# Kernel optimization log

Measured on AMD Instinct MI355X. Metric: run time of the kernel, lower is better.

The kernel has to match this reference:

```python
import jax, jax.numpy as jnp
import numpy as np

# Mixtral attention constants
H, KVH, HD = 32, 8, 128      # query heads, kv heads, head dim
WINDOW = 512                  # sliding window
THETA = 1e6                   # rope theta
B, S = 4, 1024                # batch (sequences), tokens per sequence
BS, NUM_BLOCKS = 64, 72       # paged cache block size / total blocks
DM = H * HD                   # 4096 hidden size


def rotate_half(x):
    x1, x2 = jnp.split(x, 2, axis=-1)
    return jnp.concatenate((-x2, x1), axis=-1)


def setup_inputs() -> dict:
    key = jax.random.key(0)
    ks = jax.random.split(key, 6)
    hidden_states = jax.random.normal(ks[0], (B * S, DM), dtype=jnp.float32)
    Wq = jax.random.normal(ks[1], (DM, H * HD), dtype=jnp.float32) * 0.02
    Wk = jax.random.normal(ks[2], (DM, KVH * HD), dtype=jnp.float32) * 0.02
    Wv = jax.random.normal(ks[3], (DM, KVH * HD), dtype=jnp.float32) * 0.02
    Wo = jax.random.normal(ks[4], (H * HD, DM), dtype=jnp.float32) * 0.02
    k_cache = jnp.zeros((NUM_BLOCKS, BS, KVH, HD), dtype=jnp.float32)
    v_cache = jnp.zeros((NUM_BLOCKS, BS, KVH, HD), dtype=jnp.float32)
    # identity page table: seq b owns blocks [b*16, (b+1)*16)
    block_offsets = jnp.arange(B * (S // BS), dtype=jnp.int32).reshape(B, S // BS)
    position_ids = jnp.broadcast_to(jnp.arange(S, dtype=jnp.int32)[None, :], (B, S))
    return {"hidden_states": hidden_states, "Wq": Wq, "Wk": Wk, "Wv": Wv,
            "Wo": Wo, "k_cache": k_cache, "v_cache": v_cache,
            "block_offsets": block_offsets, "position_ids": position_ids}


def reference(hidden_states, Wq, Wk, Wv, Wo, k_cache, v_cache, block_offsets, position_ids):
    b, s = position_ids.shape
    bs = k_cache.shape[1]
    nblk = s // bs
    # qkv projections (contiguous batching: tokens flattened)
    q = (hidden_states @ Wq).reshape(b, s, H, HD)
    k = (hidden_states @ Wk).reshape(b, s, KVH, HD)
    v = (hidden_states @ Wv).reshape(b, s, KVH, HD)
    # rotary embedding (rotate-half form)
    inv_freq = 1.0 / (THETA ** (jnp.arange(0, HD, 2, dtype=jnp.float32) / HD))
    freqs = position_ids.astype(jnp.float32)[..., None] * inv_freq  # [b,s,HD/2]
    emb = jnp.concatenate((freqs, freqs), axis=-1)                   # [b,s,HD]
    cos = jnp.cos(emb)[:, :, None, :]
    sin = jnp.sin(emb)[:, :, None, :]
    q = q * cos + rotate_half(q) * sin
    k = k * cos + rotate_half(k) * sin
    # paged KV-cache fill: scatter per-sequence blocks into the cache
    k_cache = k_cache.at[block_offsets].set(k.reshape(b, nblk, bs, KVH, HD))
    v_cache = v_cache.at[block_offsets].set(v.reshape(b, nblk, bs, KVH, HD))
    # paged attention: gather K/V back through the block table
    kf = k_cache[block_offsets].reshape(b, s, KVH, HD)
    vf = v_cache[block_offsets].reshape(b, s, KVH, HD)
    g = H // KVH  # GQA group size
    qg = q.reshape(b, s, KVH, g, HD)
    scores = jnp.einsum('bqhgd,bkhd->bhgqk', qg, kf) / jnp.sqrt(jnp.float32(HD))
    i = jnp.arange(s)[:, None]
    j = jnp.arange(s)[None, :]
    mask = (j <= i) & (j > i - WINDOW)  # causal + sliding window
    scores = jnp.where(mask, scores, jnp.float32(-1e30))
    probs = jax.nn.softmax(scores, axis=-1)
    out = jnp.einsum('bhgqk,bkhd->bqhgd', probs, vf).reshape(b, s, H * HD)
    return (out @ Wo).reshape(b * s, -1)
```

## Files before the change

kernel.cpp:

```cpp
#include <hip/hip_runtime.h>
#include <cstdint>

typedef __bf16 bf16_t;
typedef __attribute__((ext_vector_type(8))) __bf16 bf16x8;
typedef __attribute__((ext_vector_type(4))) __bf16 bf16x4;
typedef __attribute__((ext_vector_type(4))) float f32x4;

typedef __attribute__((address_space(1))) void void_g;
typedef __attribute__((address_space(3))) void void_l;

#define GLDS16(gp, lp) __builtin_amdgcn_global_load_lds( \
    (void_g*)(uintptr_t)(gp), (void_l*)(uintptr_t)(lp), 16, 0, 0)

constexpr int Bc = 4, Sc = 1024, Hc = 32, KVHc = 8, HDc = 128, DMc = 4096;
constexpr int NQ = 6144;
constexpr int WINc = 512;

__global__ void cast_kernel(const float* __restrict__ in, bf16_t* __restrict__ out, int n4) {
    int i = blockIdx.x * blockDim.x + threadIdx.x;
    if (i >= n4) return;
    float4 v = reinterpret_cast<const float4*>(in)[i];
    bf16x4 o;
    o[0] = (bf16_t)v.x; o[1] = (bf16_t)v.y; o[2] = (bf16_t)v.z; o[3] = (bf16_t)v.w;
    reinterpret_cast<bf16x4*>(out)[i] = o;
}

__global__ void transpose_cast(const float* __restrict__ in, bf16_t* __restrict__ out,
                               int R, int C) {
    __shared__ float tile[32][33];
    int c0 = blockIdx.x * 32, r0 = blockIdx.y * 32;
    int tx = threadIdx.x, ty = threadIdx.y;
    for (int i = 0; i < 32; i += 8)
        tile[ty + i][tx] = in[(size_t)(r0 + ty + i) * C + c0 + tx];
    __syncthreads();
    for (int i = 0; i < 32; i += 8)
        out[(size_t)(c0 + ty + i) * R + r0 + tx] = (bf16_t)tile[tx][ty + i];
}

template <typename CT>
__global__ __launch_bounds__(256) void gemm_bt(const bf16_t* __restrict__ A,
                                               const bf16_t* __restrict__ BT,
                                               CT* __restrict__ C,
                                               int M, int N, int K) {
    __shared__ bf16_t As[128 * 32];
    __shared__ bf16_t Bs[128 * 32];
    const int t = threadIdx.x;
    const int lane = t & 63, wave = t >> 6;
    const int wr = wave >> 1, wc = wave & 1;
    const int l15 = lane & 15, quad = lane >> 4;

    const int pid = blockIdx.y * gridDim.x + blockIdx.x;
    const int npn = gridDim.x, npm = gridDim.y;
    const int gsz = 8 * npn;
    const int grp = pid / gsz;
    const int first = grp * 8;
    const int gs = (npm - first) < 8 ? (npm - first) : 8;
    const int pm = first + (pid % gs);
    const int pn = (pid % gsz) / gs;
    const int mBase = pm * 128, nBase = pn * 128;

    const int srow = t >> 2;
    const int scol = (((t & 3) ^ ((srow >> 1) & 3)) * 8);
    const bf16_t* Ag = A + (size_t)(mBase + srow) * K + scol;
    const bf16_t* Bg = BT + (size_t)(nBase + srow) * K + scol;
    bf16_t* ldsA = &As[wave * 512];
    bf16_t* ldsB = &Bs[wave * 512];

    const int rsw = ((quad ^ ((l15 >> 1) & 3)) * 8);

    f32x4 acc[4][4] = {};

    for (int kk = 0; kk < K; kk += 32) {
        GLDS16(Ag + kk,                  ldsA);
        GLDS16(Ag + kk + (size_t)64 * K, ldsA + 2048);
        GLDS16(Bg + kk,                  ldsB);
        GLDS16(Bg + kk + (size_t)64 * K, ldsB + 2048);
        __syncthreads();
        bf16x8 af[4], bfv[4];
#pragma unroll
        for (int i = 0; i < 4; i++)
            af[i] = *reinterpret_cast<const bf16x8*>(&As[(wr * 64 + i * 16 + l15) * 32 + rsw]);
#pragma unroll
        for (int j = 0; j < 4; j++)
            bfv[j] = *reinterpret_cast<const bf16x8*>(&Bs[(wc * 64 + j * 16 + l15) * 32 + rsw]);
#pragma unroll
        for (int i = 0; i < 4; i++)
#pragma unroll
            for (int j = 0; j < 4; j++)
                acc[i][j] = __builtin_amdgcn_mfma_f32_16x16x32_bf16(af[i], bfv[j], acc[i][j], 0, 0, 0);
        __syncthreads();
    }
#pragma unroll
    for (int i = 0; i < 4; i++) {
        int row0 = mBase + wr * 64 + i * 16 + quad * 4;
#pragma unroll
        for (int j = 0; j < 4; j++) {
            int col = nBase + wc * 64 + j * 16 + l15;
#pragma unroll
            for (int r = 0; r < 4; r++)
                C[(size_t)(row0 + r) * N + col] = (CT)acc[i][j][r];
        }
    }
}

__global__ void rope_kernel(const bf16_t* __restrict__ qkv, const int* __restrict__ pos,
                            bf16_t* __restrict__ Qo, bf16_t* __restrict__ Ko) {
    int t = blockIdx.y;
    int hd = blockIdx.x * blockDim.x + threadIdx.x;
    int head = hd >> 6, d = hd & 63;
    float p = (float)pos[t];
    float invf = exp2f(-(float)d * (19.931568569324174f / 64.0f));
    float ang = p * invf;
    float sn, cs;
    __sincosf(ang, &sn, &cs);
    const bf16_t* src; bf16_t* dst;
    if (head < 32) {
        src = qkv + (size_t)t * NQ + head * 128 + d;
        dst = Qo + (size_t)t * DMc + head * 128 + d;
    } else {
        int kh = head - 32;
        src = qkv + (size_t)t * NQ + 4096 + kh * 128 + d;
        dst = Ko + (size_t)t * (KVHc * HDc) + kh * 128 + d;
    }
    float x1 = (float)src[0], x2 = (float)src[64];
    dst[0]  = (bf16_t)(x1 * cs - x2 * sn);
    dst[64] = (bf16_t)(x2 * cs + x1 * sn);
}

__global__ void vtrans_kernel(const bf16_t* __restrict__ qkv, bf16_t* __restrict__ Vt) {
    __shared__ bf16_t tile[32][33];
    int bh = blockIdx.z;
    int b = bh >> 3, kvh = bh & 7;
    int s0 = blockIdx.x * 32, d0 = blockIdx.y * 32;
    int tx = threadIdx.x, ty = threadIdx.y;
    for (int i = 0; i < 32; i += 8)
        tile[ty + i][tx] = qkv[(size_t)(b * Sc + s0 + ty + i) * NQ + 5120 + kvh * 128 + d0 + tx];
    __syncthreads();
    for (int i = 0; i < 32; i += 8)
        Vt[((size_t)bh * 128 + d0 + ty + i) * Sc + s0 + tx] = tile[tx][ty + i];
}

__global__ __launch_bounds__(256) void attn_kernel(const bf16_t* __restrict__ Q,
                                                   const bf16_t* __restrict__ Kk,
                                                   const bf16_t* __restrict__ Vt,
                                                   bf16_t* __restrict__ O) {
    __shared__ bf16_t Ks[2][32 * 128];
    __shared__ bf16_t Vs[2][128 * 32];
    __shared__ bf16_t Plds[4][16 * 32];
    const int bid = blockIdx.x;
    const int qt = bid & 63;
    const int kvh = (bid >> 6) & 7;
    const int b = bid >> 9;
    const int t = threadIdx.x;
    const int lane = t & 63, w = t >> 6;
    const int h = kvh * 4 + w;
    const int l15 = lane & 15, quad = lane >> 4;
    const int qb = qt * 16;

    bf16x8 qf[4];
    const bf16_t* qp = Q + (size_t)(b * Sc + qb + l15) * DMc + h * HDc + quad * 8;
#pragma unroll
    for (int c = 0; c < 4; c++) qf[c] = *reinterpret_cast<const bf16x8*>(qp + c * 32);

    const int kr0 = t >> 4;
    const int kc0 = (((t & 15) ^ (kr0 & 7)) * 8);
    const bf16_t* Kbase = Kk + (size_t)(b * Sc) * (KVHc * HDc) + kvh * HDc;
    const size_t kOff0 = (size_t)kr0 * (KVHc * HDc) + kc0;
    const size_t kOff1 = kOff0 + (size_t)16 * (KVHc * HDc);
    const int vd0 = t >> 2;
    const int vc0 = (((t & 3) ^ ((vd0 >> 1) & 3)) * 8);
    const bf16_t* Vbase = Vt + (size_t)(b * KVHc + kvh) * HDc * Sc;
    const size_t vOff0 = (size_t)vd0 * Sc + vc0;
    const size_t vOff1 = vOff0 + (size_t)64 * Sc;

    f32x4 oacc[8] = {};
    float m_r[4], l_r[4];
#pragma unroll
    for (int r = 0; r < 4; r++) { m_r[r] = -1e30f; l_r[r] = 0.f; }

    const int swl = (l15 >> 1) & 3;
    const int swk = l15 & 7;

    int lo = qb - (WINc - 1); if (lo < 0) lo = 0;
    const int kv_lo = lo & ~31;
    const int nsteps = (qb + 16 - kv_lo + 31) / 32;

    {
        const bf16_t* ks = Kbase + (size_t)kv_lo * (KVHc * HDc);
        GLDS16(ks + kOff0, &Ks[0][w * 512]);
        GLDS16(ks + kOff1, &Ks[0][2048 + w * 512]);
        const bf16_t* vs = Vbase + kv_lo;
        GLDS16(vs + vOff0, &Vs[0][w * 512]);
        GLDS16(vs + vOff1, &Vs[0][2048 + w * 512]);
    }

    int buf = 0;
    for (int s = 0; s < nsteps; s++) {
        const int kv = kv_lo + s * 32;
        __syncthreads();
        if (s + 1 < nsteps) {
            const int nb = buf ^ 1;
            const bf16_t* ks = Kbase + (size_t)(kv + 32) * (KVHc * HDc);
            GLDS16(ks + kOff0, &Ks[nb][w * 512]);
            GLDS16(ks + kOff1, &Ks[nb][2048 + w * 512]);
            const bf16_t* vs = Vbase + kv + 32;
            GLDS16(vs + vOff0, &Vs[nb][w * 512]);
            GLDS16(vs + vOff1, &Vs[nb][2048 + w * 512]);
        }
        f32x4 s0 = {}, s1 = {};
#pragma unroll
        for (int c = 0; c < 4; c++) {
            bf16x8 kf = *reinterpret_cast<const bf16x8*>(
                &Ks[buf][l15 * 128 + (((c * 4 + quad) ^ swk) * 8)]);
            s0 = __builtin_amdgcn_mfma_f32_16x16x32_bf16(qf[c], kf, s0, 0, 0, 0);
        }
#pragma unroll
        for (int c = 0; c < 4; c++) {
            bf16x8 kf = *reinterpret_cast<const bf16x8*>(
                &Ks[buf][(16 + l15) * 128 + (((c * 4 + quad) ^ swk) * 8)]);
            s1 = __builtin_amdgcn_mfma_f32_16x16x32_bf16(qf[c], kf, s1, 0, 0, 0);
        }
        const float scale = 0.08838834764831845f;
        const bool interior = (kv + 31 <= qb) && (kv >= qb - 496);
        float p0[4], p1[4], alpha[4];
#pragma unroll
        for (int r = 0; r < 4; r++) {
            float v0, v1;
            if (interior) {
                v0 = s0[r] * scale; v1 = s1[r] * scale;
            } else {
                int i = qb + quad * 4 + r;
                int j0 = kv + l15, j1 = j0 + 16;
                v0 = (j0 <= i && j0 > i - WINc) ? s0[r] * scale : -1e30f;
                v1 = (j1 <= i && j1 > i - WINc) ? s1[r] * scale : -1e30f;
            }
            float mx = fmaxf(v0, v1);
            mx = fmaxf(mx, __shfl_xor(mx, 1));
            mx = fmaxf(mx, __shfl_xor(mx, 2));
            mx = fmaxf(mx, __shfl_xor(mx, 4));
            mx = fmaxf(mx, __shfl_xor(mx, 8));
            float mnew = fmaxf(m_r[r], mx);
            alpha[r] = __expf(m_r[r] - mnew);
            m_r[r] = mnew;
            p0[r] = __expf(v0 - mnew);
            p1[r] = __expf(v1 - mnew);
            float rs = p0[r] + p1[r];
            rs += __shfl_xor(rs, 1);
            rs += __shfl_xor(rs, 2);
            rs += __shfl_xor(rs, 4);
            rs += __shfl_xor(rs, 8);
            l_r[r] = l_r[r] * alpha[r] + rs;
        }
#pragma unroll
        for (int c = 0; c < 8; c++)
#pragma unroll
            for (int r = 0; r < 4; r++)
                oacc[c][r] *= alpha[r];
#pragma unroll
        for (int r = 0; r < 4; r++) {
            int row = quad * 4 + r;
            int sw = (row >> 1) & 3;
            int g0 = l15 >> 3, g1 = 2 + (l15 >> 3);
            Plds[w][row * 32 + (((g0 ^ sw) << 3) | (l15 & 7))] = (bf16_t)p0[r];
            Plds[w][row * 32 + (((g1 ^ sw) << 3) | (l15 & 7))] = (bf16_t)p1[r];
        }
        bf16x8 pf = *reinterpret_cast<const bf16x8*>(&Plds[w][l15 * 32 + ((quad ^ swl) * 8)]);
#pragma unroll
        for (int c = 0; c < 8; c++) {
            bf16x8 vf = *reinterpret_cast<const bf16x8*>(
                &Vs[buf][(c * 16 + l15) * 32 + ((quad ^ swl) * 8)]);
            oacc[c] = __builtin_amdgcn_mfma_f32_16x16x32_bf16(pf, vf, oacc[c], 0, 0, 0);
        }
        buf ^= 1;
    }
    bf16_t* op = O + (size_t)(b * Sc + qb) * DMc + h * HDc;
#pragma unroll
    for (int r = 0; r < 4; r++) {
        float inv = 1.0f / l_r[r];
        int row = quad * 4 + r;
#pragma unroll
        for (int c = 0; c < 8; c++)
            op[(size_t)row * DMc + c * 16 + l15] = (bf16_t)(oacc[c][r] * inv);
    }
}

extern "C" void kernel_launch(void* const* d_in, const int* in_sizes, int n_in,
                              void* d_out, int out_size, void* d_ws, size_t ws_size,
                              hipStream_t stream) {
    const float* hidden = (const float*)d_in[0];
    const float* Wq = (const float*)d_in[1];
    const float* Wk = (const float*)d_in[2];
    const float* Wv = (const float*)d_in[3];
    const float* Wo = (const float*)d_in[4];
    const int* pos = (const int*)d_in[8];
    float* out = (float*)d_out;

    char* ws = (char*)d_ws;
    bf16_t* Abf  = (bf16_t*)(ws);
    bf16_t* B1T  = (bf16_t*)(ws + 33554432);
    bf16_t* Qo   = (bf16_t*)(ws + 33554432);
    bf16_t* Ko   = (bf16_t*)(ws + 67108864);
    bf16_t* Vt   = (bf16_t*)(ws + 75497472);
    bf16_t* WoT  = (bf16_t*)(ws + 83886080);
    bf16_t* qkv  = (bf16_t*)(ws + 117440512);
    bf16_t* attn = Abf;

    dim3 tb(32, 8);
    cast_kernel<<<16384, 256, 0, stream>>>(hidden, Abf, 4194304);
    transpose_cast<<<dim3(128, 128), tb, 0, stream>>>(Wq, B1T, 4096, 4096);
    transpose_cast<<<dim3(32, 128), tb, 0, stream>>>(Wk, B1T + (size_t)4096 * 4096, 4096, 1024);
    transpose_cast<<<dim3(32, 128), tb, 0, stream>>>(Wv, B1T + (size_t)5120 * 4096, 4096, 1024);
    transpose_cast<<<dim3(128, 128), tb, 0, stream>>>(Wo, WoT, 4096, 4096);

    gemm_bt<bf16_t><<<dim3(48, 32), 256, 0, stream>>>(Abf, B1T, qkv, 4096, 6144, 4096);

    rope_kernel<<<dim3(10, 4096), 256, 0, stream>>>(qkv, pos, Qo, Ko);
    vtrans_kernel<<<dim3(32, 4, 32), tb, 0, stream>>>(qkv, Vt);

    attn_kernel<<<2048, 256, 0, stream>>>(Qo, Ko, Vt, attn);

    gemm_bt<float><<<dim3(32, 32), 256, 0, stream>>>(attn, WoT, out, 4096, 4096, 4096);
}
```

Before: 901.7 us.

## Replace GEMM with 256x128-tile double-buffered pipelined kernel using 8 waves

```diff
diff --git a/kernel.cpp b/kernel.cpp
--- a/kernel.cpp
+++ b/kernel.cpp
@@ -38,15 +38,16 @@
 }
 
 template <typename CT>
-__global__ __launch_bounds__(256) void gemm_bt(const bf16_t* __restrict__ A,
-                                               const bf16_t* __restrict__ BT,
-                                               CT* __restrict__ C,
-                                               int M, int N, int K) {
-    __shared__ bf16_t As[128 * 32];
-    __shared__ bf16_t Bs[128 * 32];
+__global__ __launch_bounds__(512, 2) void gemm256(const bf16_t* __restrict__ A,
+                                                  const bf16_t* __restrict__ BT,
+                                                  CT* __restrict__ C,
+                                                  int M, int N, int K) {
+    __shared__ bf16_t As[2 * 2 * 256 * 32];
+    __shared__ bf16_t Bs[2 * 2 * 128 * 32];
+
     const int t = threadIdx.x;
-    const int lane = t & 63, wave = t >> 6;
-    const int wr = wave >> 1, wc = wave & 1;
+    const int lane = t & 63, w = t >> 6;
+    const int wm = w >> 2, wn = w & 3;
     const int l15 = lane & 15, quad = lane >> 4;
 
     const int pid = blockIdx.y * gridDim.x + blockIdx.x;
@@ -57,48 +58,91 @@
     const int gs = (npm - first) < 8 ? (npm - first) : 8;
     const int pm = first + (pid % gs);
     const int pn = (pid % gsz) / gs;
-    const int mBase = pm * 128, nBase = pn * 128;
-
-    const int srow = t >> 2;
-    const int scol = (((t & 3) ^ ((srow >> 1) & 3)) * 8);
-    const bf16_t* Ag = A + (size_t)(mBase + srow) * K + scol;
-    const bf16_t* Bg = BT + (size_t)(nBase + srow) * K + scol;
-    bf16_t* ldsA = &As[wave * 512];
-    bf16_t* ldsB = &Bs[wave * 512];
-
-    const int rsw = ((quad ^ ((l15 >> 1) & 3)) * 8);
-
-    f32x4 acc[4][4] = {};
-
-    for (int kk = 0; kk < K; kk += 32) {
-        GLDS16(Ag + kk,                  ldsA);
-        GLDS16(Ag + kk + (size_t)64 * K, ldsA + 2048);
-        GLDS16(Bg + kk,                  ldsB);
-        GLDS16(Bg + kk + (size_t)64 * K, ldsB + 2048);
-        __syncthreads();
-        bf16x8 af[4], bfv[4];
-#pragma unroll
-        for (int i = 0; i < 4; i++)
-            af[i] = *reinterpret_cast<const bf16x8*>(&As[(wr * 64 + i * 16 + l15) * 32 + rsw]);
-#pragma unroll
-        for (int j = 0; j < 4; j++)
-            bfv[j] = *reinterpret_cast<const bf16x8*>(&Bs[(wc * 64 + j * 16 + l15) * 32 + rsw]);
-#pragma unroll
-        for (int i = 0; i < 4; i++)
-#pragma unroll
-            for (int j = 0; j < 4; j++)
-                acc[i][j] = __builtin_amdgcn_mfma_f32_16x16x32_bf16(af[i], bfv[j], acc[i][j], 0, 0, 0);
-        __syncthreads();
-    }
-#pragma unroll
-    for (int i = 0; i < 4; i++) {
-        int row0 = mBase + wr * 64 + i * 16 + quad * 4;
-#pragma unroll
-        for (int j = 0; j < 4; j++) {
-            int col = nBase + wc * 64 + j * 16 + l15;
+    const int mBase = pm * 256, nBase = pn * 128;
+
+    const int r_in = lane >> 2;
+    const int sl = lane & 3;
+    const int g = sl ^ ((r_in >> 1) & 3);
+    const bf16_t* srcA0 = A + (size_t)(mBase + w * 16 + r_in) * K + g * 8;
+    const bf16_t* srcA1 = srcA0 + (size_t)128 * K;
+    const bf16_t* srcB0 = BT + (size_t)(nBase + w * 16 + r_in) * K + g * 8;
+
+    const int rsw = (quad ^ ((l15 >> 1) & 3)) * 8;
+    const int aoff = (wm * 128 + l15) * 32 + rsw;
+    const int boff = (wn * 32 + l15) * 32 + rsw;
+
+    f32x4 acc[8][2] = {};
+    const int NT = K >> 6;
+
+    GLDS16(srcB0,      &Bs[(0 * 128 + w * 16) * 32]);
+    GLDS16(srcA0,      &As[(0 * 256 + w * 16) * 32]);
+    GLDS16(srcA1,      &As[(0 * 256 + 128 + w * 16) * 32]);
+    GLDS16(srcB0 + 32, &Bs[(1 * 128 + w * 16) * 32]);
+    GLDS16(srcA0 + 32, &As[(1 * 256 + w * 16) * 32]);
+    GLDS16(srcA1 + 32, &As[(1 * 256 + 128 + w * 16) * 32]);
+
+    for (int ti = 0; ti < NT - 1; ++ti) {
+        const int buf = ti & 1, nbuf = buf ^ 1;
+        const size_t kk = (size_t)(ti + 1) * 64;
+#pragma unroll
+        for (int ks = 0; ks < 2; ks++) {
+            asm volatile("s_waitcnt vmcnt(3)" ::: "memory");
+            __builtin_amdgcn_s_barrier();
+            GLDS16(srcB0 + kk + ks * 32, &Bs[((nbuf * 2 + ks) * 128 + w * 16) * 32]);
+            GLDS16(srcA0 + kk + ks * 32, &As[((nbuf * 2 + ks) * 256 + w * 16) * 32]);
+            GLDS16(srcA1 + kk + ks * 32, &As[((nbuf * 2 + ks) * 256 + 128 + w * 16) * 32]);
+            bf16x8 af[8], bv[2];
+            const bf16_t* Ab = &As[(buf * 2 + ks) * 8192 + aoff];
+            const bf16_t* Bb = &Bs[(buf * 2 + ks) * 4096 + boff];
+#pragma unroll
+            for (int mf = 0; mf < 8; mf++)
+                af[mf] = *reinterpret_cast<const bf16x8*>(Ab + mf * 512);
+#pragma unroll
+            for (int nf = 0; nf < 2; nf++)
+                bv[nf] = *reinterpret_cast<const bf16x8*>(Bb + nf * 512);
+            __builtin_amdgcn_s_setprio(1);
+#pragma unroll
+            for (int mf = 0; mf < 8; mf++)
+#pragma unroll
+                for (int nf = 0; nf < 2; nf++)
+                    acc[mf][nf] = __builtin_amdgcn_mfma_f32_16x16x32_bf16(af[mf], bv[nf], acc[mf][nf], 0, 0, 0);
+            __builtin_amdgcn_s_setprio(0);
+        }
+    }
+    {
+        const int buf = (NT - 1) & 1;
+#pragma unroll
+        for (int ks = 0; ks < 2; ks++) {
+            if (ks == 0) { asm volatile("s_waitcnt vmcnt(3)" ::: "memory"); }
+            else         { asm volatile("s_waitcnt vmcnt(0)" ::: "memory"); }
+            __builtin_amdgcn_s_barrier();
+            bf16x8 af[8], bv[2];
+            const bf16_t* Ab = &As[(buf * 2 + ks) * 8192 + aoff];
+            const bf16_t* Bb = &Bs[(buf * 2 + ks) * 4096 + boff];
+#pragma unroll
+            for (int mf = 0; mf < 8; mf++)
+                af[mf] = *reinterpret_cast<const bf16x8*>(Ab + mf * 512);
+#pragma unroll
+            for (int nf = 0; nf < 2; nf++)
+                bv[nf] = *reinterpret_cast<const bf16x8*>(Bb + nf * 512);
+            __builtin_amdgcn_s_setprio(1);
+#pragma unroll
+            for (int mf = 0; mf < 8; mf++)
+#pragma unroll
+                for (int nf = 0; nf < 2; nf++)
+                    acc[mf][nf] = __builtin_amdgcn_mfma_f32_16x16x32_bf16(af[mf], bv[nf], acc[mf][nf], 0, 0, 0);
+            __builtin_amdgcn_s_setprio(0);
+        }
+    }
+#pragma unroll
+    for (int mf = 0; mf < 8; mf++) {
+        const int row0 = mBase + wm * 128 + mf * 16 + quad * 4;
+#pragma unroll
+        for (int nf = 0; nf < 2; nf++) {
+            const int col = nBase + wn * 32 + nf * 16 + l15;
 #pragma unroll
             for (int r = 0; r < 4; r++)
-                C[(size_t)(row0 + r) * N + col] = (CT)acc[i][j][r];
+                C[(size_t)(row0 + r) * N + col] = (CT)acc[mf][nf][r];
         }
     }
 }
@@ -312,12 +356,12 @@
     transpose_cast<<<dim3(32, 128), tb, 0, stream>>>(Wv, B1T + (size_t)5120 * 4096, 4096, 1024);
     transpose_cast<<<dim3(128, 128), tb, 0, stream>>>(Wo, WoT, 4096, 4096);
 
-    gemm_bt<bf16_t><<<dim3(48, 32), 256, 0, stream>>>(Abf, B1T, qkv, 4096, 6144, 4096);
+    gemm256<bf16_t><<<dim3(48, 16), 512, 0, stream>>>(Abf, B1T, qkv, 4096, 6144, 4096);
 
     rope_kernel<<<dim3(10, 4096), 256, 0, stream>>>(qkv, pos, Qo, Ko);
     vtrans_kernel<<<dim3(32, 4, 32), tb, 0, stream>>>(qkv, Vt);
 
     attn_kernel<<<2048, 256, 0, stream>>>(Qo, Ko, Vt, attn);
 
-    gemm_bt<float><<<dim3(32, 32), 256, 0, stream>>>(attn, WoT, out, 4096, 4096, 4096);
-}
+    gemm256<float><<<dim3(32, 16), 512, 0, stream>>>(attn, WoT, out, 4096, 4096, 4096);
+}
```

Result: faster. 782.8 us (-13.2%).

## Replace GEMM with 256x256-tile multi-stage pipelined LDS kernel

Applied to the files above, without the earlier changes.

```diff
diff --git a/kernel.cpp b/kernel.cpp
--- a/kernel.cpp
+++ b/kernel.cpp
@@ -38,15 +38,16 @@
 }
 
 template <typename CT>
-__global__ __launch_bounds__(256) void gemm_bt(const bf16_t* __restrict__ A,
-                                               const bf16_t* __restrict__ BT,
-                                               CT* __restrict__ C,
-                                               int M, int N, int K) {
-    __shared__ bf16_t As[128 * 32];
-    __shared__ bf16_t Bs[128 * 32];
+__global__ __launch_bounds__(512, 2) void gemm256(const bf16_t* __restrict__ A,
+                                                  const bf16_t* __restrict__ BT,
+                                                  CT* __restrict__ C,
+                                                  int M, int N, int K) {
+    __shared__ bf16_t As[4][256 * 32];
+    __shared__ bf16_t Bs[4][256 * 32];
+
     const int t = threadIdx.x;
-    const int lane = t & 63, wave = t >> 6;
-    const int wr = wave >> 1, wc = wave & 1;
+    const int lane = t & 63, w = t >> 6;
+    const int wm = w >> 2, wn = w & 3;
     const int l15 = lane & 15, quad = lane >> 4;
 
     const int pid = blockIdx.y * gridDim.x + blockIdx.x;
@@ -57,48 +58,80 @@
     const int gs = (npm - first) < 8 ? (npm - first) : 8;
     const int pm = first + (pid % gs);
     const int pn = (pid % gsz) / gs;
-    const int mBase = pm * 128, nBase = pn * 128;
-
-    const int srow = t >> 2;
-    const int scol = (((t & 3) ^ ((srow >> 1) & 3)) * 8);
-    const bf16_t* Ag = A + (size_t)(mBase + srow) * K + scol;
-    const bf16_t* Bg = BT + (size_t)(nBase + srow) * K + scol;
-    bf16_t* ldsA = &As[wave * 512];
-    bf16_t* ldsB = &Bs[wave * 512];
-
-    const int rsw = ((quad ^ ((l15 >> 1) & 3)) * 8);
-
-    f32x4 acc[4][4] = {};
-
-    for (int kk = 0; kk < K; kk += 32) {
-        GLDS16(Ag + kk,                  ldsA);
-        GLDS16(Ag + kk + (size_t)64 * K, ldsA + 2048);
-        GLDS16(Bg + kk,                  ldsB);
-        GLDS16(Bg + kk + (size_t)64 * K, ldsB + 2048);
-        __syncthreads();
-        bf16x8 af[4], bfv[4];
-#pragma unroll
-        for (int i = 0; i < 4; i++)
-            af[i] = *reinterpret_cast<const bf16x8*>(&As[(wr * 64 + i * 16 + l15) * 32 + rsw]);
-#pragma unroll
-        for (int j = 0; j < 4; j++)
-            bfv[j] = *reinterpret_cast<const bf16x8*>(&Bs[(wc * 64 + j * 16 + l15) * 32 + rsw]);
-#pragma unroll
-        for (int i = 0; i < 4; i++)
-#pragma unroll
-            for (int j = 0; j < 4; j++)
-                acc[i][j] = __builtin_amdgcn_mfma_f32_16x16x32_bf16(af[i], bfv[j], acc[i][j], 0, 0, 0);
-        __syncthreads();
-    }
-#pragma unroll
-    for (int i = 0; i < 4; i++) {
-        int row0 = mBase + wr * 64 + i * 16 + quad * 4;
-#pragma unroll
-        for (int j = 0; j < 4; j++) {
-            int col = nBase + wc * 64 + j * 16 + l15;
-#pragma unroll
-            for (int r = 0; r < 4; r++)
-                C[(size_t)(row0 + r) * N + col] = (CT)acc[i][j][r];
+    const int mBase = pm * 256, nBase = pn * 256;
+
+    const int srow = lane >> 2;
+    const int sg = (lane & 3) ^ ((srow >> 1) & 3);
+    const int rL0 = w * 16 + srow;
+    const int rL1 = 128 + w * 16 + srow;
+    const bf16_t* pA0 = A + (size_t)(mBase + rL0) * K + sg * 8;
+    const bf16_t* pA1 = A + (size_t)(mBase + rL1) * K + sg * 8;
+    const bf16_t* pB0 = BT + (size_t)(nBase + rL0) * K + sg * 8;
+    const bf16_t* pB1 = BT + (size_t)(nBase + rL1) * K + sg * 8;
+    const int dstL0 = w * 512;
+    const int dstL1 = 4096 + w * 512;
+
+    const int swz = (quad ^ ((l15 >> 1) & 3)) * 8;
+    const int rdA = (wm * 128 + l15) * 32 + swz;
+    const int rdB = (wn * 64 + l15) * 32 + swz;
+
+    f32x4 acc[8][4] = {};
+    const int NT = K >> 5;
+
+#pragma unroll
+    for (int u = 0; u < 3; ++u) {
+        const size_t kk = (size_t)u * 32;
+        GLDS16(pA0 + kk, &As[u][dstL0]);
+        GLDS16(pA1 + kk, &As[u][dstL1]);
+        GLDS16(pB0 + kk, &Bs[u][dstL0]);
+        GLDS16(pB1 + kk, &Bs[u][dstL1]);
+    }
+
+#define GBODY(VMC, DOSTAGE) do {                                              \
+    const int buf = tt & 3;                                                   \
+    asm volatile("s_waitcnt vmcnt(" #VMC ")" ::: "memory");                   \
+    __builtin_amdgcn_s_barrier();                                             \
+    __builtin_amdgcn_sched_barrier(0);                                        \
+    if (DOSTAGE) {                                                            \
+        const int ub = (tt + 3) & 3;                                          \
+        const size_t kk = (size_t)(tt + 3) * 32;                              \
+        GLDS16(pA0 + kk, &As[ub][dstL0]);                                     \
+        GLDS16(pA1 + kk, &As[ub][dstL1]);                                     \
+        GLDS16(pB0 + kk, &Bs[ub][dstL0]);                                     \
+        GLDS16(pB1 + kk, &Bs[ub][dstL1]);                                     \
+    }                                                                         \
+    bf16x8 af[8], bv[4];                                                      \
+    _Pragma("unroll")                                                         \
+    for (int mf = 0; mf < 8; ++mf)                                            \
+        af[mf] = *reinterpret_cast<const bf16x8*>(&As[buf][rdA + mf * 512]);  \
+    _Pragma("unroll")                                                         \
+    for (int nf = 0; nf < 4; ++nf)                                            \
+        bv[nf] = *reinterpret_cast<const bf16x8*>(&Bs[buf][rdB + nf * 512]);  \
+    __builtin_amdgcn_s_setprio(1);                                            \
+    _Pragma("unroll")                                                         \
+    for (int mf = 0; mf < 8; ++mf)                                            \
+        _Pragma("unroll")                                                     \
+        for (int nf = 0; nf < 4; ++nf)                                        \
+            acc[mf][nf] = __builtin_amdgcn_mfma_f32_16x16x32_bf16(            \
+                af[mf], bv[nf], acc[mf][nf], 0, 0, 0);                        \
+    __builtin_amdgcn_s_setprio(0);                                            \
+} while (0)
+
+    for (int tt = 0; tt < NT - 3; ++tt) GBODY(8, true);
+    { const int tt = NT - 3; GBODY(8, false); }
+    { const int tt = NT - 2; GBODY(4, false); }
+    { const int tt = NT - 1; GBODY(0, false); }
+#undef GBODY
+
+#pragma unroll
+    for (int mf = 0; mf < 8; ++mf) {
+        const int row0 = mBase + wm * 128 + mf * 16 + quad * 4;
+#pragma unroll
+        for (int nf = 0; nf < 4; ++nf) {
+            const int col = nBase + wn * 64 + nf * 16 + l15;
+#pragma unroll
+            for (int r = 0; r < 4; ++r)
+                C[(size_t)(row0 + r) * N + col] = (CT)acc[mf][nf][r];
         }
     }
 }
@@ -312,12 +345,12 @@
     transpose_cast<<<dim3(32, 128), tb, 0, stream>>>(Wv, B1T + (size_t)5120 * 4096, 4096, 1024);
     transpose_cast<<<dim3(128, 128), tb, 0, stream>>>(Wo, WoT, 4096, 4096);
 
-    gemm_bt<bf16_t><<<dim3(48, 32), 256, 0, stream>>>(Abf, B1T, qkv, 4096, 6144, 4096);
+    gemm256<bf16_t><<<dim3(24, 16), 512, 0, stream>>>(Abf, B1T, qkv, 4096, 6144, 4096);
 
     rope_kernel<<<dim3(10, 4096), 256, 0, stream>>>(qkv, pos, Qo, Ko);
     vtrans_kernel<<<dim3(32, 4, 32), tb, 0, stream>>>(qkv, Vt);
 
     attn_kernel<<<2048, 256, 0, stream>>>(Qo, Ko, Vt, attn);
 
-    gemm_bt<float><<<dim3(32, 32), 256, 0, stream>>>(attn, WoT, out, 4096, 4096, 4096);
-}
+    gemm256<float><<<dim3(16, 16), 512, 0, stream>>>(attn, WoT, out, 4096, 4096, 4096);
+}
```

After: 756.1 us. -16.1%, faster.
